# Kernel tuning notes

Measured on AMD Instinct MI355X. Metric: run time of the kernel, lower is better.

## Reference

```python
import jax, jax.numpy as jnp
import numpy as np

L = 4          # num_layers
H = 512        # hidden_size == input_size
B, S = 8, 4096
LN_EPS = 1e-5


def parallel_scan_log(coeffs, values):
    """h_t = coeffs_t * h_{t-1} + values_t via Hillis-Steele log-step scan.
    coeffs, values: (B, S, H). Faithful to the torch loop incl. clamp."""
    seq_len = coeffs.shape[1]
    a = jnp.clip(coeffs, 1e-08, 1.0 - 1e-08)
    b = values
    num_steps = int(seq_len - 1).bit_length()
    for step in range(num_steps):
        d = 1 << step
        if d >= seq_len:
            break
        a_prev = jnp.pad(a[:, :-d, :], ((0, 0), (d, 0), (0, 0)), constant_values=1.0)
        b_prev = jnp.pad(b[:, :-d, :], ((0, 0), (d, 0), (0, 0)), constant_values=0.0)
        b = a * b_prev + b   # uses old a (matches a_new/b_new then assign)
        a = a * a_prev
    return b


def mingru_layer(x, Wz, bz, Wh, bh):
    # x: (B,S,in) ; Wz,Wh: (H,in) torch Linear layout (y = x @ W.T + b)
    z = jax.nn.sigmoid(jnp.einsum('bsi,hi->bsh', x, Wz) + bz)
    h_tilde = jnp.tanh(jnp.einsum('bsi,hi->bsh', x, Wh) + bh)
    return parallel_scan_log(1.0 - z, z * h_tilde)


def layer_norm(x, g, b):
    mu = jnp.mean(x, axis=-1, keepdims=True)
    var = jnp.mean(jnp.square(x - mu), axis=-1, keepdims=True)
    return (x - mu) * jax.lax.rsqrt(var + LN_EPS) * g + b


def run_layers(x, Wz, bz, Wh, bh, ln_g, ln_b):
    h = x
    for i in range(L):
        h_new = mingru_layer(h, Wz[i], bz[i], Wh[i], bh[i])
        if i > 0:
            h_new = h_new + h  # residual (shapes match for i>0)
        h = layer_norm(h_new, ln_g, ln_b)  # dropout==Identity (p=0)
    return h


def setup_inputs() -> dict:
    key = jax.random.key(0)
    ks = jax.random.split(key, 12)
    lim = 1.0 / np.sqrt(H)  # torch Linear default init range
    u = lambda k, shp: jax.random.uniform(k, shp, jnp.float32, -lim, lim)
    return {
        'x': jax.random.normal(ks[0], (B, S, H), jnp.float32),
        'Wz_f': u(ks[1], (L, H, H)), 'bz_f': u(ks[2], (L, H)),
        'Wh_f': u(ks[3], (L, H, H)), 'bh_f': u(ks[4], (L, H)),
        'Wz_b': u(ks[5], (L, H, H)), 'bz_b': u(ks[6], (L, H)),
        'Wh_b': u(ks[7], (L, H, H)), 'bh_b': u(ks[8], (L, H)),
        'fusion_w': u(ks[9], (H, 2 * H)), 'fusion_b': u(ks[10], (H,)),
        'ln_g': jnp.ones((H,), jnp.float32), 'ln_b': jnp.zeros((H,), jnp.float32),
    }


def reference(x, Wz_f, bz_f, Wh_f, bh_f, Wz_b, bz_b, Wh_b, bh_b, fusion_w, fusion_b, ln_g, ln_b):
    out_fwd = run_layers(x, Wz_f, bz_f, Wh_f, bh_f, ln_g, ln_b)
    x_rev = jnp.flip(x, axis=1)
    out_bwd = jnp.flip(run_layers(x_rev, Wz_b, bz_b, Wh_b, bh_b, ln_g, ln_b), axis=1)
    out_comb = jnp.concatenate([out_fwd, out_bwd], axis=-1)  # (B,S,2H)
    return jnp.einsum('bsk,hk->bsh', out_comb, fusion_w) + fusion_b
```

## Files before the change

### kernel.cpp

```cpp
#include <hip/hip_runtime.h>

#define HID 512
#define SLEN 4096
#define NB 8
#define BSROWS (NB*SLEN)
#define NLAYER 4
#define CHUNKT 128
#define NCHUNK 32
#define MTPD 256
#define CGALL 8192

typedef float f32x4 __attribute__((ext_vector_type(4)));
typedef unsigned int u32x4 __attribute__((ext_vector_type(4)));

typedef const __attribute__((address_space(1))) unsigned int* gas_u32p;
typedef __attribute__((address_space(3))) unsigned int* las_u32p;

__device__ __forceinline__ float bf2f(unsigned short u){
  union { unsigned int i; float f; } v; v.i = ((unsigned int)u) << 16; return v.f;
}
__device__ __forceinline__ unsigned short f2bf(float f){
  union { float f; unsigned int i; } v; v.f = f;
  unsigned int u = v.i;
  u = u + 0x7fffu + ((u >> 16) & 1u);
  return (unsigned short)(u >> 16);
}
__device__ __forceinline__ void mfma_bf16(f32x4& acc, u32x4 a, u32x4 b){
  asm("v_mfma_f32_16x16x32_bf16 %0, %1, %2, %0" : "+v"(acc) : "v"(a), "v"(b));
}
__device__ __forceinline__ void mfma_fence(){
  __builtin_amdgcn_sched_barrier(0);
  asm volatile("s_nop 7\n\ts_nop 7\n\ts_nop 7\n\ts_nop 7");
  __builtin_amdgcn_sched_barrier(0);
}
__device__ __forceinline__ void decode_ab(unsigned int v, float& a, float& b){
  a = (float)(v & 0xffffu) * (1.f/65535.f);
  b = fmaf((float)(v >> 16), 2.f/65535.f, -1.f);
}
__device__ __forceinline__ void gload_lds16(const unsigned short* g, unsigned short* l){
  __builtin_amdgcn_global_load_lds((gas_u32p)(const void*)g, (las_u32p)(void*)l, 16, 0, 0);
}
__device__ __forceinline__ int scidx(int row, int col){
  return row*64 + (col ^ (((row>>2)&3)<<4));
}


__global__ __launch_bounds__(256) void prep_all(
    const float* __restrict__ wzf, const float* __restrict__ whf,
    const float* __restrict__ wzb, const float* __restrict__ whb,
    const float* __restrict__ fw,  const float* __restrict__ x,
    unsigned short* __restrict__ wbf, unsigned short* __restrict__ outw,
    unsigned short* __restrict__ X0)
{
  int idx = blockIdx.x*256 + threadIdx.x;
  const float* p;
  unsigned short* q;
  if (idx < 524288){
    int i8  = idx & 63;
    int o   = (idx >> 6) & 511;
    int m   = (idx >> 15) & 1;
    int l   = (idx >> 16) & 3;
    int dir = idx >> 18;
    const float* src = dir ? (m ? whb : wzb) : (m ? whf : wzf);
    p = src + ((size_t)(l*512 + o)*512 + i8*8);
    q = wbf + ((((size_t)(dir*4 + l)*2 + m)*512 + o)*512 + i8*8);
  } else if (idx < 589824){
    int j = idx - 524288;
    p = fw + (size_t)j*8;
    q = outw + (size_t)j*8;
  } else {
    int j = idx - 589824;
    p = x + (size_t)j*8;
    q = X0 + (size_t)j*8;
  }
  float4 v0 = *(const float4*)p;
  float4 v1 = *(const float4*)(p+4);
  u32x4 outv;
  outv[0] = (unsigned)f2bf(v0.x) | ((unsigned)f2bf(v0.y)<<16);
  outv[1] = (unsigned)f2bf(v0.z) | ((unsigned)f2bf(v0.w)<<16);
  outv[2] = (unsigned)f2bf(v1.x) | ((unsigned)f2bf(v1.y)<<16);
  outv[3] = (unsigned)f2bf(v1.z) | ((unsigned)f2bf(v1.w)<<16);
  *(u32x4*)q = outv;
}


__global__ __launch_bounds__(256, 4) void gate_gemm_scan(
    const unsigned short* __restrict__ X,
    const unsigned short* __restrict__ Wbf,
    const float* __restrict__ bzf, const float* __restrict__ bhf,
    const float* __restrict__ bzb, const float* __restrict__ bhb,
    unsigned int* __restrict__ PH0,
    unsigned int* __restrict__ PH1,
    float* __restrict__ Aagg, float* __restrict__ Bagg,
    int layer, int xoff1, int flip1)
{
  __shared__ __align__(16) unsigned char smem[32768 + 2048];
  unsigned short* As  = (unsigned short*)smem;
  unsigned short* Bzs = (unsigned short*)(smem + 16384);
  unsigned short* Bhs = (unsigned short*)(smem + 24576);
  unsigned int*   SC  = (unsigned int*)smem;
  float* SegP = (float*)(smem + 32768);
  float* SegH = (float*)(smem + 32768 + 1024);

  int hw = blockIdx.x;
  int dir = hw >= (MTPD*8);
  int hwl = hw - dir*(MTPD*8);
  int lg = (hwl & 7)*MTPD + (hwl >> 3);
  int nt  = lg & 7;
  int mt  = lg >> 3;

  const unsigned short* Xp = X + (size_t)(dir ? xoff1 : 0)*512;
  const int flip = dir ? flip1 : 0;
  const unsigned short* Wz = Wbf + ((size_t)((dir*4 + layer)*2 + 0))*(512*512);
  const unsigned short* Wh = Wbf + ((size_t)((dir*4 + layer)*2 + 1))*(512*512);
  const float* bzp = (dir ? bzb : bzf) + layer*512;
  const float* bhp = (dir ? bhb : bhf) + layer*512;
  unsigned int* PHp = dir ? PH1 : PH0;

  const int tid = threadIdx.x;
  const int lane = tid & 63;
  const int wv = tid >> 6;
  const int n0 = nt*64;
  const int slot = tid & 7;
  const int rowb = tid >> 3;

  f32x4 accz[2][4], acch[2][4];
  #pragma unroll
  for (int i=0;i<2;++i)
    #pragma unroll
    for (int j=0;j<4;++j){ accz[i][j] = (f32x4)(0.f); acch[i][j] = (f32x4)(0.f); }

  for (int ks=0; ks<8; ++ks){
    int k0 = ks*64;
    #pragma unroll
    for (int it=0; it<4; ++it){
      int row = rowb + it*32;
      int sr = (mt*128 + row) ^ flip;
      u32x4 v = *(const u32x4*)(Xp + (size_t)sr*512 + k0 + slot*8);
      *(u32x4*)(As + row*64 + ((slot ^ (row&7))<<3)) = v;
    }
    #pragma unroll
    for (int it=0; it<2; ++it){
      int row = rowb + it*32;
      u32x4 vz = *(const u32x4*)(Wz + (size_t)(n0+row)*512 + k0 + slot*8);
      *(u32x4*)(Bzs + row*64 + ((slot ^ (row&7))<<3)) = vz;
      u32x4 vh = *(const u32x4*)(Wh + (size_t)(n0+row)*512 + k0 + slot*8);
      *(u32x4*)(Bhs + row*64 + ((slot ^ (row&7))<<3)) = vh;
    }
    __syncthreads();
    #pragma unroll
    for (int kk=0; kk<2; ++kk){
      int kslot = kk*4 + (lane >> 4);
      u32x4 af[2];
      #pragma unroll
      for (int mf=0; mf<2; ++mf){
        int row = wv*32 + mf*16 + (lane & 15);
        af[mf] = *(const u32x4*)(As + row*64 + ((kslot ^ (row&7))<<3));
      }
      #pragma unroll
      for (int nf=0; nf<4; ++nf){
        int row = nf*16 + (lane & 15);
        u32x4 bz = *(const u32x4*)(Bzs + row*64 + ((kslot ^ (row&7))<<3));
        u32x4 bh = *(const u32x4*)(Bhs + row*64 + ((kslot ^ (row&7))<<3));
        #pragma unroll
        for (int mf=0; mf<2; ++mf){
          mfma_bf16(accz[mf][nf], af[mf], bz);
          mfma_bf16(acch[mf][nf], af[mf], bh);
        }
      }
    }
    __syncthreads();
  }
  mfma_fence();

  const float C1 = 1.44269504f;
  const float C2 = 2.88539008f;
  #pragma unroll
  for (int nf=0; nf<4; ++nf){
    int colL = nf*16 + (lane & 15);
    float bz = bzp[n0 + colL];
    float bh = bhp[n0 + colL];
    #pragma unroll
    for (int mf=0; mf<2; ++mf){
      int rloc = wv*32 + mf*16 + ((lane>>4)<<2);
      #pragma unroll
      for (int r=0; r<4; ++r){
        float zp = accz[mf][nf][r] + bz;
        float hp = acch[mf][nf][r] + bh;
        float a  = __builtin_amdgcn_rcpf(1.f + __builtin_amdgcn_exp2f(C1*zp));
        float th = fmaf(-2.f, __builtin_amdgcn_rcpf(1.f + __builtin_amdgcn_exp2f(C2*hp)), 1.f);
        a = fminf(fmaxf(a, 1e-8f), 1.0f);
        float bv = fmaf(-a, th, th);
        unsigned aq = (unsigned)fmaf(a, 65535.f, 0.5f);
        unsigned bq = (unsigned)fmaf(bv, 32767.5f, 32768.0f);
        SC[scidx(rloc + r, colL)] = aq | (bq << 16);
      }
    }
  }
  __syncthreads();

  const int col = tid & 63;
  const int seg = tid >> 6;
  float ar[32], br[32];
  {
    float P = 1.f, Hl = 0.f;
    #pragma unroll
    for (int r=0; r<32; ++r){
      float a, b; decode_ab(SC[scidx(seg*32 + r, col)], a, b);
      ar[r] = a; br[r] = b;
      Hl = fmaf(a, Hl, b);
      P *= a;
    }
    SegP[seg*64 + col] = P;
    SegH[seg*64 + col] = Hl;
  }
  __syncthreads();

  float Ppre = 1.f, Hpre = 0.f;
  for (int j=0; j<seg; ++j){
    Hpre = fmaf(SegP[j*64 + col], Hpre, SegH[j*64 + col]);
    Ppre *= SegP[j*64 + col];
  }

  const int rowbase = mt*128;
  float pl = 1.f, hl = 0.f;
  float Pg = 1.f, Hg = 0.f;
  #pragma unroll
  for (int r=0; r<32; ++r){
    hl = fmaf(ar[r], hl, br[r]);
    pl *= ar[r];
    Pg = Ppre * pl;
    Hg = fmaf(pl, Hpre, hl);
    unsigned pq = (unsigned)fmaf(Pg, 65535.f, 0.5f);
    PHp[(size_t)(rowbase + seg*32 + r)*512 + n0 + col] = pq | ((unsigned)f2bf(Hg) << 16);
  }
  if (seg == 3){
    int chain = dir*4096 + (mt >> 5)*512 + n0 + col;
    int c = mt & 31;
    Aagg[c*CGALL + chain] = Pg;
    Bagg[c*CGALL + chain] = Hg;
  }
}


__global__ __launch_bounds__(256) void scan_p2(
    const float* __restrict__ Aagg, const float* __restrict__ Bagg,
    float* __restrict__ Hin)
{
  int chain = blockIdx.x*256 + threadIdx.x;
  float hv = 0.f;
  #pragma unroll
  for (int c=0; c<NCHUNK; ++c){
    Hin[c*CGALL + chain] = hv;
    hv = fmaf(Aagg[c*CGALL + chain], hv, Bagg[c*CGALL + chain]);
  }
}


__global__ __launch_bounds__(256) void recon_ln(
    const unsigned int* __restrict__ PH0,
    const unsigned int* __restrict__ PH1,
    const float* __restrict__ Hin,
    unsigned short* __restrict__ Xio,
    const float* __restrict__ g, const float* __restrict__ bta, int resid)
{
  int token = blockIdx.x*4 + (threadIdx.x >> 6);
  int lane = threadIdx.x & 63;
  int dir  = token >> 15;
  int tloc = token & (BSROWS-1);
  const unsigned int* PHp = dir ? PH1 : PH0;
  size_t pbase = (size_t)tloc*512 + lane*8;
  u32x4 p0 = *(const u32x4*)(PHp + pbase);
  u32x4 p1 = *(const u32x4*)(PHp + pbase + 4);
  int c = (tloc >> 7) & 31;
  const float* hin = Hin + (size_t)c*CGALL + (token >> 12)*512 + lane*8;
  f32x4 h0 = *(const f32x4*)hin;
  f32x4 h1 = *(const f32x4*)(hin + 4);
  float v[8];
  #pragma unroll
  for (int j=0; j<4; ++j){
    v[j]   = fmaf((float)(p0[j] & 0xffffu)*(1.f/65535.f), h0[j], bf2f((unsigned short)(p0[j] >> 16)));
    v[4+j] = fmaf((float)(p1[j] & 0xffffu)*(1.f/65535.f), h1[j], bf2f((unsigned short)(p1[j] >> 16)));
  }
  size_t base = (size_t)token*512 + lane*8;
  if (resid){
    u32x4 xv = *(const u32x4*)(Xio + base);
    #pragma unroll
    for (int w=0; w<4; ++w){
      v[2*w]   += bf2f((unsigned short)(xv[w] & 0xffffu));
      v[2*w+1] += bf2f((unsigned short)(xv[w] >> 16));
    }
  }
  float s = 0.f, s2 = 0.f;
  #pragma unroll
  for (int j=0; j<8; ++j){ s += v[j]; s2 += v[j]*v[j]; }
  #pragma unroll
  for (int o=1; o<64; o<<=1){ s += __shfl_xor(s, o, 64); s2 += __shfl_xor(s2, o, 64); }
  float mu = s * (1.f/512.f);
  float var = s2 * (1.f/512.f) - mu*mu;
  float inv = rsqrtf(var + 1e-5f);
  float4 g0 = *(const float4*)(g + lane*8);
  float4 g1 = *(const float4*)(g + lane*8 + 4);
  float4 b0 = *(const float4*)(bta + lane*8);
  float4 b1 = *(const float4*)(bta + lane*8 + 4);
  float gg[8]  = {g0.x,g0.y,g0.z,g0.w,g1.x,g1.y,g1.z,g1.w};
  float bbv[8] = {b0.x,b0.y,b0.z,b0.w,b1.x,b1.y,b1.z,b1.w};
  u32x4 outv;
  #pragma unroll
  for (int w=0; w<4; ++w){
    float y0 = (v[2*w]   - mu)*inv*gg[2*w]   + bbv[2*w];
    float y1 = (v[2*w+1] - mu)*inv*gg[2*w+1] + bbv[2*w+1];
    outv[w] = (unsigned)f2bf(y0) | ((unsigned)f2bf(y1) << 16);
  }
  *(u32x4*)(Xio + base) = outv;
}


__global__ __launch_bounds__(256, 4) void fusion_gemm(
    const unsigned short* __restrict__ Xf,
    const unsigned short* __restrict__ Wf,
    const float* __restrict__ fb,
    float* __restrict__ outp)
{
  __shared__ __align__(16) unsigned short As[128*64];
  __shared__ __align__(16) unsigned short Bs[64*64];

  int hw = blockIdx.x;
  int lg = (hw & 7)*256 + (hw >> 3);
  int nt = lg & 7;
  int mt = lg >> 3;

  const int tid = threadIdx.x;
  const int lane = tid & 63;
  const int wv = tid >> 6;
  const int n0 = nt*64;
  const int lrow  = lane >> 3;
  const int slotp = (lane & 7) ^ (lrow & 7);

  f32x4 acc[2][4];
  #pragma unroll
  for (int i=0;i<2;++i)
    #pragma unroll
    for (int j=0;j<4;++j) acc[i][j] = (f32x4)(0.f);

  for (int ks=0; ks<16; ++ks){
    int k0 = ks*64;
    const unsigned short* Abase = Xf + ((k0 >= 512) ? (size_t)BSROWS*512 : 0);
    int kc = k0 & 511;
    int flip = (k0 >= 512) ? 4095 : 0;
    #pragma unroll
    for (int it=0; it<4; ++it){
      int row = it*32 + wv*8 + lrow;
      int sr = (mt*128 + row) ^ flip;
      gload_lds16(Abase + (size_t)sr*512 + kc + slotp*8,
                  As + (it*32 + wv*8)*64);
    }
    #pragma unroll
    for (int it=0; it<2; ++it){
      int row = it*32 + wv*8 + lrow;
      gload_lds16(Wf + (size_t)(n0 + row)*1024 + k0 + slotp*8,
                  Bs + (it*32 + wv*8)*64);
    }
    __syncthreads();
    #pragma unroll
    for (int kk=0; kk<2; ++kk){
      int kslot = kk*4 + (lane >> 4);
      u32x4 af[2];
      #pragma unroll
      for (int mf=0; mf<2; ++mf){
        int row = wv*32 + mf*16 + (lane & 15);
        af[mf] = *(const u32x4*)(As + row*64 + ((kslot ^ (row&7))<<3));
      }
      #pragma unroll
      for (int nf=0; nf<4; ++nf){
        int row = nf*16 + (lane & 15);
        u32x4 bv = *(const u32x4*)(Bs + row*64 + ((kslot ^ (row&7))<<3));
        #pragma unroll
        for (int mf=0; mf<2; ++mf) mfma_bf16(acc[mf][nf], af[mf], bv);
      }
    }
    __syncthreads();
  }
  mfma_fence();

  #pragma unroll
  for (int nf=0; nf<4; ++nf){
    int col = n0 + nf*16 + (lane & 15);
    float bias = fb[col];
    #pragma unroll
    for (int mf=0; mf<2; ++mf){
      int rb = mt*128 + wv*32 + mf*16 + ((lane>>4)<<2);
      #pragma unroll
      for (int r=0; r<4; ++r)
        outp[(size_t)(rb + r)*512 + col] = acc[mf][nf][r] + bias;
    }
  }
}


extern "C" void kernel_launch(void* const* d_in, const int* in_sizes, int n_in,
                              void* d_out, int out_size, void* d_ws, size_t ws_size,
                              hipStream_t stream)
{
  (void)in_sizes; (void)n_in; (void)out_size; (void)ws_size;
  const float* x   = (const float*)d_in[0];
  const float* wzf = (const float*)d_in[1];
  const float* bzf = (const float*)d_in[2];
  const float* whf = (const float*)d_in[3];
  const float* bhf = (const float*)d_in[4];
  const float* wzb = (const float*)d_in[5];
  const float* bzb = (const float*)d_in[6];
  const float* whb = (const float*)d_in[7];
  const float* bhb = (const float*)d_in[8];
  const float* fw  = (const float*)d_in[9];
  const float* fbb = (const float*)d_in[10];
  const float* lng = (const float*)d_in[11];
  const float* lnb = (const float*)d_in[12];
  float* outp = (float*)d_out;

  char* ws = (char*)d_ws;
  size_t o = 0;
  unsigned short* Wbf = (unsigned short*)(ws + o); o += (size_t)16*512*512*2;
  unsigned short* Wfb = (unsigned short*)(ws + o); o += (size_t)512*1024*2;
  unsigned short* X   = (unsigned short*)(ws + o); o += (size_t)2*BSROWS*512*2;
  unsigned int*   PH0 = (unsigned int*)  (ws + o); o += (size_t)BSROWS*512*4;
  float* Aagg = (float*)(ws + o); o += (size_t)CGALL*NCHUNK*4;
  float* Bagg = (float*)(ws + o); o += (size_t)CGALL*NCHUNK*4;
  float* Hin  = (float*)(ws + o); o += (size_t)CGALL*NCHUNK*4;
  unsigned int* PH1 = (unsigned int*)d_out;

  prep_all<<<10496, 256, 0, stream>>>(wzf, whf, wzb, whb, fw, x, Wbf, Wfb, X);

  for (int l = 0; l < NLAYER; ++l){
    int xoff1 = (l == 0) ? 0 : BSROWS;
    int flip1 = (l == 0) ? 4095 : 0;
    gate_gemm_scan<<<4096, 256, 0, stream>>>(X, Wbf, bzf, bhf, bzb, bhb,
                                             PH0, PH1, Aagg, Bagg, l, xoff1, flip1);
    scan_p2 <<<CGALL/256, 256, 0, stream>>>(Aagg, Bagg, Hin);
    recon_ln<<<16384, 256, 0, stream>>>(PH0, PH1, Hin, X, lng, lnb, l > 0 ? 1 : 0);
  }

  fusion_gemm<<<2048, 256, 0, stream>>>(X, Wfb, fbb, outp);
}
```

Baseline: 600.4 us.

## Double gate GEMM M-tile to 256 rows with 512-thread blocks

The fused gate GEMM+scan kernel now gives each block 256 sequence rows instead of 128, using 512 threads and twice the shared memory. The goal is to halve the number of weight-tile loads per output and the block count, amortising W staging. The in-block scan is split into two 128-row halves, each writing its own chunk aggregate. This keeps the chunk layout for the cross-chunk pass. The larger LDS footprint (about 68KB per block) limits how many blocks fit per CU, which may reduce latency hiding.

Measured after the change: 619.2 us. 1.03x slower.

```diff
diff --git a/kernel.cpp b/kernel.cpp
--- a/kernel.cpp
+++ b/kernel.cpp
@@ -7,7 +7,7 @@
 #define NLAYER 4
 #define CHUNKT 128
 #define NCHUNK 32
-#define MTPD 256
+#define MT256 128
 #define CGALL 8192
 
 typedef float f32x4 __attribute__((ext_vector_type(4)));
@@ -84,7 +84,7 @@
 }
 
 
-__global__ __launch_bounds__(256, 4) void gate_gemm_scan(
+__global__ __launch_bounds__(512, 4) void gate_gemm_scan(
     const unsigned short* __restrict__ X,
     const unsigned short* __restrict__ Wbf,
     const float* __restrict__ bzf, const float* __restrict__ bhf,
@@ -94,18 +94,18 @@
     float* __restrict__ Aagg, float* __restrict__ Bagg,
     int layer, int xoff1, int flip1)
 {
-  __shared__ __align__(16) unsigned char smem[32768 + 2048];
+  __shared__ __align__(16) unsigned char smem[65536 + 4096];
   unsigned short* As  = (unsigned short*)smem;
-  unsigned short* Bzs = (unsigned short*)(smem + 16384);
-  unsigned short* Bhs = (unsigned short*)(smem + 24576);
+  unsigned short* Bzs = (unsigned short*)(smem + 32768);
+  unsigned short* Bhs = (unsigned short*)(smem + 40960);
   unsigned int*   SC  = (unsigned int*)smem;
-  float* SegP = (float*)(smem + 32768);
-  float* SegH = (float*)(smem + 32768 + 1024);
+  float* SegP = (float*)(smem + 65536);
+  float* SegH = (float*)(smem + 65536 + 2048);
 
   int hw = blockIdx.x;
-  int dir = hw >= (MTPD*8);
-  int hwl = hw - dir*(MTPD*8);
-  int lg = (hwl & 7)*MTPD + (hwl >> 3);
+  int dir = hw >= (MT256*8);
+  int hwl = hw - dir*(MT256*8);
+  int lg = (hwl & 7)*MT256 + (hwl >> 3);
   int nt  = lg & 7;
   int mt  = lg >> 3;
 
@@ -134,14 +134,13 @@
     int k0 = ks*64;
     #pragma unroll
     for (int it=0; it<4; ++it){
-      int row = rowb + it*32;
-      int sr = (mt*128 + row) ^ flip;
+      int row = rowb + it*64;
+      int sr = (mt*256 + row) ^ flip;
       u32x4 v = *(const u32x4*)(Xp + (size_t)sr*512 + k0 + slot*8);
       *(u32x4*)(As + row*64 + ((slot ^ (row&7))<<3)) = v;
     }
-    #pragma unroll
-    for (int it=0; it<2; ++it){
-      int row = rowb + it*32;
+    {
+      int row = rowb;
       u32x4 vz = *(const u32x4*)(Wz + (size_t)(n0+row)*512 + k0 + slot*8);
       *(u32x4*)(Bzs + row*64 + ((slot ^ (row&7))<<3)) = vz;
       u32x4 vh = *(const u32x4*)(Wh + (size_t)(n0+row)*512 + k0 + slot*8);
@@ -201,12 +200,14 @@
 
   const int col = tid & 63;
   const int seg = tid >> 6;
+  const int half = seg >> 2;
+  const int rbase = half*128 + (seg & 3)*32;
   float ar[32], br[32];
   {
     float P = 1.f, Hl = 0.f;
     #pragma unroll
     for (int r=0; r<32; ++r){
-      float a, b; decode_ab(SC[scidx(seg*32 + r, col)], a, b);
+      float a, b; decode_ab(SC[scidx(rbase + r, col)], a, b);
       ar[r] = a; br[r] = b;
       Hl = fmaf(a, Hl, b);
       P *= a;
@@ -217,12 +218,12 @@
   __syncthreads();
 
   float Ppre = 1.f, Hpre = 0.f;
-  for (int j=0; j<seg; ++j){
+  for (int j = half*4; j < seg; ++j){
     Hpre = fmaf(SegP[j*64 + col], Hpre, SegH[j*64 + col]);
     Ppre *= SegP[j*64 + col];
   }
 
-  const int rowbase = mt*128;
+  const int growbase = mt*256 + rbase;
   float pl = 1.f, hl = 0.f;
   float Pg = 1.f, Hg = 0.f;
   #pragma unroll
@@ -232,11 +233,12 @@
     Pg = Ppre * pl;
     Hg = fmaf(pl, Hpre, hl);
     unsigned pq = (unsigned)fmaf(Pg, 65535.f, 0.5f);
-    PHp[(size_t)(rowbase + seg*32 + r)*512 + n0 + col] = pq | ((unsigned)f2bf(Hg) << 16);
-  }
-  if (seg == 3){
-    int chain = dir*4096 + (mt >> 5)*512 + n0 + col;
-    int c = mt & 31;
+    PHp[(size_t)(growbase + r)*512 + n0 + col] = pq | ((unsigned)f2bf(Hg) << 16);
+  }
+  if ((seg & 3) == 3){
+    int cg = mt*2 + half;
+    int chain = dir*4096 + (cg >> 5)*512 + n0 + col;
+    int c = cg & 31;
     Aagg[c*CGALL + chain] = Pg;
     Bagg[c*CGALL + chain] = Hg;
   }
@@ -434,7 +436,7 @@
   for (int l = 0; l < NLAYER; ++l){
     int xoff1 = (l == 0) ? 0 : BSROWS;
     int flip1 = (l == 0) ? 4095 : 0;
-    gate_gemm_scan<<<4096, 256, 0, stream>>>(X, Wbf, bzf, bhf, bzb, bhb,
+    gate_gemm_scan<<<2048, 512, 0, stream>>>(X, Wbf, bzf, bhf, bzb, bhb,
                                              PH0, PH1, Aagg, Bagg, l, xoff1, flip1);
     scan_p2 <<<CGALL/256, 256, 0, stream>>>(Aagg, Bagg, Hin);
     recon_ln<<<16384, 256, 0, stream>>>(PH0, PH1, Hin, X, lng, lnb, l > 0 ? 1 : 0);
```
